# Optimization experiments

Measured on AMD Instinct MI355X. Metric: run time of the kernel, lower is better.

Reference implementation:

```python
import jax, jax.numpy as jnp
import numpy as np

N = 50000          # nodes
E = 800000         # edges per metapath
P = 4              # metapaths
IN = 256           # in_size
D = 32 * 8         # out_size * layer_num_heads = 256
SEM_H = 128        # SemanticAttention hidden


def setup_inputs() -> dict:
    key = jax.random.key(0)
    ks = jax.random.split(key, 8)
    h = jax.random.normal(ks[0], (N, IN), dtype=jnp.float32)
    src = jax.random.randint(ks[1], (P, E), 0, N, dtype=jnp.int32)
    dst = jax.random.randint(ks[2], (P, E), 0, N, dtype=jnp.int32)
    # per-metapath GraphConv weights (Glorot-ish scale)
    W_gc = jax.random.normal(ks[3], (P, IN, D), dtype=jnp.float32) / np.sqrt(IN)
    b_gc = jnp.zeros((P, D), dtype=jnp.float32)
    # SemanticAttention: Linear(D, SEM_H) -> tanh -> Linear(SEM_H, 1, bias=False)
    W1 = jax.random.normal(ks[4], (D, SEM_H), dtype=jnp.float32) / np.sqrt(D)
    b1 = jnp.zeros((SEM_H,), dtype=jnp.float32)
    w2 = jax.random.normal(ks[5], (SEM_H,), dtype=jnp.float32) / np.sqrt(SEM_H)
    return {"h": h, "src": src, "dst": dst, "W_gc": W_gc, "b_gc": b_gc,
            "W1": W1, "b1": b1, "w2": w2}


def _graph_conv(h, src, dst, W, b):
    # DGL GraphConv with norm='both': D_dst^{-1/2} A D_src^{-1/2} (h W) + b
    ones = jnp.ones((src.shape[0],), dtype=h.dtype)
    deg_out = jnp.clip(jax.ops.segment_sum(ones, src, num_segments=N), 1.0)
    deg_in = jnp.clip(jax.ops.segment_sum(ones, dst, num_segments=N), 1.0)
    x = (h @ W) * jax.lax.rsqrt(deg_out)[:, None]          # [N, D]
    agg = jax.ops.segment_sum(x[src], dst, num_segments=N)  # gather-scatter [N, D]
    return agg * jax.lax.rsqrt(deg_in)[:, None] + b


def reference(h, src, dst, W_gc, b_gc, W1, b1, w2):
    # per-metapath GraphConv (fixed small loop over P metapaths)
    zs = [_graph_conv(h, src[p], dst[p], W_gc[p], b_gc[p]) for p in range(P)]
    z = jnp.stack(zs, axis=1)                               # [N, P, D]
    # SemanticAttention: project -> mean over nodes -> softmax over metapaths
    s = jnp.tanh(z @ W1 + b1) @ w2                          # [N, P]
    beta = jax.nn.softmax(s.mean(axis=0), axis=0)           # [P]
    return jnp.einsum('npd,p->nd', z, beta)                 # [N, D]
```

## Files before the change

kernel.cpp:

```cpp
#include <hip/hip_runtime.h>

#define NN 50000
#define NE 800000
#define NP 4
#define DIN 256
#define DD 256
#define NH 128
#define SA 40
#define NSEG 16
#define SEGE (NE / NSEG)
#define HCH 32768
#define NHC 2
#define SCH 8192
#define NSC 7
#define SPAD(k) ((k) + ((k) >> 5))

typedef __attribute__((ext_vector_type(8))) short bf16x8;
typedef __attribute__((ext_vector_type(4))) float f32x4;
typedef __attribute__((ext_vector_type(2))) float f32x2;

__device__ __forceinline__ unsigned short f2bf(float f) {
  unsigned u = __float_as_uint(f);
  u += 0x7fff + ((u >> 16) & 1);
  return (unsigned short)(u >> 16);
}
__device__ __forceinline__ float bfl(unsigned u) { return __uint_as_float(u << 16); }
__device__ __forceinline__ float bfh(unsigned u) { return __uint_as_float(u & 0xffff0000u); }


__global__ __launch_bounds__(256) void histX_kernel(const int* __restrict__ src,
                                                    const int* __restrict__ dst,
                                                    ushort* __restrict__ cntS,
                                                    ushort* __restrict__ cntD) {
  __shared__ int hs[HCH];
  int bx = blockIdx.x;
  int c = bx % NHC, s = bx / NHC;
  int p = blockIdx.y;
  const int* idx = blockIdx.z ? dst : src;
  ushort* cnt = blockIdx.z ? cntD : cntS;
  int base = c * HCH, nk = min(HCH, NN - base);
  for (int k = threadIdx.x; k < HCH; k += 256) hs[k] = 0;
  __syncthreads();
  const int4* a4 = (const int4*)(idx + (size_t)p * NE + (size_t)s * SEGE);
  for (int i = threadIdx.x; i < SEGE / 4; i += 256) {
    int4 v = a4[i];
    int k;
    k = v.x - base; if ((unsigned)k < (unsigned)nk) atomicAdd(&hs[k], 1);
    k = v.y - base; if ((unsigned)k < (unsigned)nk) atomicAdd(&hs[k], 1);
    k = v.z - base; if ((unsigned)k < (unsigned)nk) atomicAdd(&hs[k], 1);
    k = v.w - base; if ((unsigned)k < (unsigned)nk) atomicAdd(&hs[k], 1);
  }
  __syncthreads();
  ushort* out = cnt + (size_t)(p * NSEG + s) * NN + base;
  for (int k = threadIdx.x; k < nk; k += 256) out[k] = (ushort)hs[k];
}


__global__ __launch_bounds__(1024) void scanA_kernel(
    ushort* __restrict__ cntD, const ushort* __restrict__ cntS,
    float* __restrict__ rin, float* __restrict__ rout,
    int* __restrict__ row_ptr, int* __restrict__ chunkdeg) {
  int c = blockIdx.x, p = blockIdx.y;
  int base = c * SCH, nk = min(SCH, NN - base);
  __shared__ int sdeg[SCH + (SCH >> 5)];
  __shared__ int wtot[16], wexc[16];
  int t = threadIdx.x;
  for (int kk = t; kk < SCH; kk += 1024) {
    int run = 0;
    if (kk < nk) {
      size_t o = (size_t)(p * NSEG) * NN + base + kk;
      int vD[NSEG], vS[NSEG];
#pragma unroll
      for (int s = 0; s < NSEG; ++s) vD[s] = cntD[o + (size_t)s * NN];
#pragma unroll
      for (int s = 0; s < NSEG; ++s) vS[s] = cntS[o + (size_t)s * NN];
#pragma unroll
      for (int s = 0; s < NSEG; ++s) {
        cntD[o + (size_t)s * NN] = (ushort)run;
        run += vD[s];
      }
      int rs = 0;
#pragma unroll
      for (int s = 0; s < NSEG; ++s) rs += vS[s];
      rin[(size_t)p * NN + base + kk] = rsqrtf((float)max(run, 1));
      rout[(size_t)p * NN + base + kk] = rsqrtf((float)max(rs, 1));
    }
    sdeg[SPAD(kk)] = run;
  }
  __syncthreads();
  int loc[8];
  int ssum = 0;
#pragma unroll
  for (int j = 0; j < 8; ++j) { loc[j] = ssum; ssum += sdeg[SPAD(t * 8 + j)]; }
  int incl = ssum;
  int lane = t & 63, w = t >> 6;
#pragma unroll
  for (int o = 1; o < 64; o <<= 1) {
    int v = __shfl_up(incl, o);
    if (lane >= o) incl += v;
  }
  if (lane == 63) wtot[w] = incl;
  __syncthreads();
  if (t == 0) {
    int r = 0;
    for (int i = 0; i < 16; ++i) { wexc[i] = r; r += wtot[i]; }
  }
  __syncthreads();
  int tbase = wexc[w] + incl - ssum;
  int* rp = row_ptr + (size_t)p * (NN + 1) + base;
#pragma unroll
  for (int j = 0; j < 8; ++j) {
    int k = t * 8 + j;
    if (k < nk) rp[k] = tbase + loc[j];
  }
  if (t == 1023) chunkdeg[p * NSC + c] = tbase + ssum;
}


__global__ __launch_bounds__(1024) void rpfin_kernel(int* __restrict__ row_ptr,
                                                     const int* __restrict__ chunkdeg) {
  int k = blockIdx.x * 1024 + threadIdx.x, p = blockIdx.y;
  if (k < NN) {
    int c = k >> 13;
    int cb = 0;
    for (int i = 0; i < c; ++i) cb += chunkdeg[p * NSC + i];
    row_ptr[(size_t)p * (NN + 1) + k] += cb;
  }
  if (k == 0) row_ptr[(size_t)p * (NN + 1) + NN] = NE;
}


__global__ __launch_bounds__(256) void scatter_kernel(
    const int* __restrict__ src, const int* __restrict__ dst,
    const ushort* __restrict__ cntD, const int* __restrict__ row_ptr, int* __restrict__ col) {
  __shared__ int cur[HCH];
  int bx = blockIdx.x;
  int c = bx % NHC, s = bx / NHC;
  int p = blockIdx.y;
  int base = c * HCH, nk = min(HCH, NN - base);
  for (int k = threadIdx.x; k < nk; k += 256)
    cur[k] = row_ptr[(size_t)p * (NN + 1) + base + k] +
             cntD[(size_t)(p * NSEG + s) * NN + base + k];
  __syncthreads();
  const int4* d4 = (const int4*)(dst + (size_t)p * NE + (size_t)s * SEGE);
  const int4* s4 = (const int4*)(src + (size_t)p * NE + (size_t)s * SEGE);
  int* colp = col + (size_t)p * NE;
  for (int i = threadIdx.x; i < SEGE / 4; i += 256) {
    int4 dv = d4[i];
    int4 sv = s4[i];
    int k;
    k = dv.x - base; if ((unsigned)k < (unsigned)nk) colp[atomicAdd(&cur[k], 1)] = sv.x;
    k = dv.y - base; if ((unsigned)k < (unsigned)nk) colp[atomicAdd(&cur[k], 1)] = sv.y;
    k = dv.z - base; if ((unsigned)k < (unsigned)nk) colp[atomicAdd(&cur[k], 1)] = sv.z;
    k = dv.w - base; if ((unsigned)k < (unsigned)nk) colp[atomicAdd(&cur[k], 1)] = sv.w;
  }
}


__global__ void cvt_h_kernel(const float4* __restrict__ h4, ushort4* __restrict__ h2) {
  int i = blockIdx.x * blockDim.x + threadIdx.x;
  if (i >= NN * DIN / 4) return;
  float4 v = h4[i];
  ushort4 o;
  o.x = f2bf(v.x); o.y = f2bf(v.y); o.z = f2bf(v.z); o.w = f2bf(v.w);
  h2[i] = o;
}


__global__ __launch_bounds__(256) void agg_kernel(
    const ushort* __restrict__ h2, const int* __restrict__ col,
    const int* __restrict__ row_ptr, const float* __restrict__ rout,
    const float* __restrict__ rin, ushort* __restrict__ g, int pbase) {
  __shared__ int2 sW[4][64];
  int p = pbase + blockIdx.y;
  int v = blockIdx.x * 4 + (threadIdx.x >> 6);
  int lane = threadIdx.x & 63;
  int wv = threadIdx.x >> 6;
  const int* colp = col + (size_t)p * NE;
  const float* rop = rout + (size_t)p * NN;
  int beg = row_ptr[p * (NN + 1) + v], end = row_ptr[p * (NN + 1) + v + 1];
  const char* hb = (const char*)h2 + (size_t)lane * 8;
  f32x2 accA0 = {0.f, 0.f}, accA1 = {0.f, 0.f};
  f32x2 accB0 = {0.f, 0.f}, accB1 = {0.f, 0.f};
  for (int j0 = beg; j0 < end; j0 += 64) {
    int nw = end - j0;
    if (nw > 64) nw = 64;
    int cv = 0;
    float rv = 0.f;
    if (lane < nw) { cv = colp[j0 + lane]; rv = rop[cv]; }
    sW[wv][lane] = make_int2(cv, __float_as_int(rv));
    int nwb = (nw + 7) & ~7;
    for (int t = 0; t < nwb; t += 8) {
      int2 w[8];
#pragma unroll
      for (int q = 0; q < 8; ++q) w[q] = sW[wv][t + q];
      uint2 u[8];
#pragma unroll
      for (int q = 0; q < 8; ++q)
        u[q] = *(const uint2*)(hb + ((size_t)(unsigned)w[q].x << 9));
#pragma unroll
      for (int q = 0; q < 8; ++q) {
        float r = __int_as_float(w[q].y);
        f32x2 rr = {r, r};
        if (q & 1) {
          asm("v_pk_fma_f32 %0, %1, %2, %0" : "+v"(accB0) : "v"(rr), "v"((f32x2){bfl(u[q].x), bfh(u[q].x)}));
          asm("v_pk_fma_f32 %0, %1, %2, %0" : "+v"(accB1) : "v"(rr), "v"((f32x2){bfl(u[q].y), bfh(u[q].y)}));
        } else {
          asm("v_pk_fma_f32 %0, %1, %2, %0" : "+v"(accA0) : "v"(rr), "v"((f32x2){bfl(u[q].x), bfh(u[q].x)}));
          asm("v_pk_fma_f32 %0, %1, %2, %0" : "+v"(accA1) : "v"(rr), "v"((f32x2){bfl(u[q].y), bfh(u[q].y)}));
        }
      }
    }
  }
  float ri = rin[(size_t)p * NN + v];
  f32x2 s0 = accA0 + accB0;
  f32x2 s1 = accA1 + accB1;
  ushort4 o;
  o.x = f2bf(s0.x * ri); o.y = f2bf(s0.y * ri);
  o.z = f2bf(s1.x * ri); o.w = f2bf(s1.y * ri);
  ((ushort4*)(g + ((size_t)p * NN + v) * DIN))[lane] = o;
}


__global__ void wmulcvec_kernel(const float* __restrict__ Wgc, const float* __restrict__ bgc,
                                const float* __restrict__ W1, const float* __restrict__ b1,
                                ushort* __restrict__ Mt, float* __restrict__ cvec) {
  int p = blockIdx.y, k = blockIdx.x, j = threadIdx.x;
  if (k < DIN) {
    const float* wrow = Wgc + ((size_t)p * DIN + k) * DD;
    float s = 0.f;
    for (int d = 0; d < DD; ++d) s = fmaf(wrow[d], W1[(size_t)d * NH + j], s);
    Mt[((size_t)p * NH + j) * DIN + k] = f2bf(s);
  } else {
    const float* b = bgc + (size_t)p * DD;
    float s = b1[j];
    for (int d = 0; d < DD; ++d) s = fmaf(b[d], W1[(size_t)d * NH + j], s);
    cvec[p * NH + j] = s;
  }
}


__global__ __launch_bounds__(256) void gemm_sem(
    const ushort* __restrict__ g, const ushort* __restrict__ Mt,
    const float* __restrict__ cvec, const float* __restrict__ w2,
    float* __restrict__ ssum) {
  __shared__ ushort As[128 * SA];
  __shared__ ushort Bs[128 * SA];
  __shared__ float wsumf[4];
  const int tid = threadIdx.x;
  const int p = blockIdx.y;
  const int row0 = blockIdx.x * 128;
  const int wave = tid >> 6, lane = tid & 63;
  const int wr = wave >> 1, wc = wave & 1;
  const int q = tid >> 2, sseg = tid & 3;
  const int srow = ((q & 31) << 1) | (q >> 5);
  const int fr = lane & 15, fk = (lane >> 4) * 8;
  const ushort* Ag = g + (size_t)p * NN * DIN;
  const ushort* Bg = Mt + (size_t)p * NH * DIN;
  int ar0 = row0 + srow; if (ar0 >= NN) ar0 = NN - 1;
  int ar1 = row0 + srow + 64; if (ar1 >= NN) ar1 = NN - 1;
  f32x4 acc[4][4] = {};
  for (int k2 = 0; k2 < DIN; k2 += 32) {
    uint4 av0 = *(const uint4*)(Ag + (size_t)ar0 * DIN + k2 + sseg * 8);
    uint4 av1 = *(const uint4*)(Ag + (size_t)ar1 * DIN + k2 + sseg * 8);
    uint4 bv0 = *(const uint4*)(Bg + (size_t)srow * DIN + k2 + sseg * 8);
    uint4 bv1 = *(const uint4*)(Bg + (size_t)(srow + 64) * DIN + k2 + sseg * 8);
    __syncthreads();
    *(uint4*)&As[srow * SA + sseg * 8] = av0;
    *(uint4*)&As[(srow + 64) * SA + sseg * 8] = av1;
    *(uint4*)&Bs[srow * SA + sseg * 8] = bv0;
    *(uint4*)&Bs[(srow + 64) * SA + sseg * 8] = bv1;
    __syncthreads();
    bf16x8 af[4], bfv[4];
#pragma unroll
    for (int t = 0; t < 4; ++t) {
      af[t] = *(const bf16x8*)&As[(wr * 64 + t * 16 + fr) * SA + fk];
      bfv[t] = *(const bf16x8*)&Bs[(wc * 64 + t * 16 + fr) * SA + fk];
    }
#pragma unroll
    for (int mt = 0; mt < 4; ++mt)
#pragma unroll
      for (int nt = 0; nt < 4; ++nt)
        acc[mt][nt] = __builtin_amdgcn_mfma_f32_16x16x32_bf16(af[mt], bfv[nt], acc[mt][nt], 0, 0, 0);
  }
  float s = 0.f;
#pragma unroll
  for (int nt = 0; nt < 4; ++nt) {
    int c = wc * 64 + nt * 16 + fr;
    float cc = cvec[p * NH + c];
    float ww = w2[c];
#pragma unroll
    for (int mt = 0; mt < 4; ++mt)
#pragma unroll
      for (int i = 0; i < 4; ++i) {
        int r = row0 + wr * 64 + mt * 16 + (lane >> 4) * 4 + i;
        if (r < NN) {
          float x = acc[mt][nt][i] + cc;
          x = fminf(fmaxf(x, -15.f), 15.f);
          float e = __expf(2.f * x);
          s = fmaf((e - 1.f) / (e + 1.f), ww, s);
        }
      }
  }
#pragma unroll
  for (int o = 32; o > 0; o >>= 1) s += __shfl_down(s, o);
  if (lane == 0) wsumf[wave] = s;
  __syncthreads();
  if (tid == 0) atomicAdd(&ssum[p], wsumf[0] + wsumf[1] + wsumf[2] + wsumf[3]);
}


__global__ __launch_bounds__(256) void scaleWtB_kernel(const float* __restrict__ Wgc,
                                                       const float* __restrict__ ssum,
                                                       const float* __restrict__ bgc,
                                                       ushort* __restrict__ Wt,
                                                       float* __restrict__ bout) {
  float m[NP];
  float mx = -1e30f;
#pragma unroll
  for (int p = 0; p < NP; ++p) {
    m[p] = ssum[p] * (1.f / (float)NN);
    mx = fmaxf(mx, m[p]);
  }
  float tot = 0.f;
#pragma unroll
  for (int p = 0; p < NP; ++p) { m[p] = __expf(m[p] - mx); tot += m[p]; }
  float inv = 1.f / tot;
  if (blockIdx.x == 0) {
    int d = threadIdx.x;
    float s = 0.f;
#pragma unroll
    for (int p = 0; p < NP; ++p) s = fmaf(m[p] * inv, bgc[p * DD + d], s);
    bout[d] = s;
  }
  int i = blockIdx.x * 256 + threadIdx.x;
  if (i < DD * NP * DIN) {
    int n = i >> 10;
    int pk = i & 1023;
    int p = pk >> 8, k = pk & 255;
    Wt[i] = f2bf(m[p] * inv * Wgc[((size_t)p * DIN + k) * DD + n]);
  }
}


__global__ __launch_bounds__(256) void gemm_main(
    const ushort* __restrict__ g, const ushort* __restrict__ Wt,
    const float* __restrict__ bout, float* __restrict__ out) {
  __shared__ ushort As[128 * SA];
  __shared__ ushort Bs[128 * SA];
  const int tid = threadIdx.x;
  const int row0 = blockIdx.y * 128;
  const int col0 = blockIdx.x * 128;
  const int wave = tid >> 6, lane = tid & 63;
  const int wr = wave >> 1, wc = wave & 1;
  const int q = tid >> 2, sseg = tid & 3;
  const int srow = ((q & 31) << 1) | (q >> 5);
  const int fr = lane & 15, fk = (lane >> 4) * 8;
  int ar0 = row0 + srow; if (ar0 >= NN) ar0 = NN - 1;
  int ar1 = row0 + srow + 64; if (ar1 >= NN) ar1 = NN - 1;
  f32x4 acc[4][4] = {};
  for (int p = 0; p < NP; ++p) {
    const ushort* Ag = g + (size_t)p * NN * DIN;
    for (int k2 = 0; k2 < DIN; k2 += 32) {
      uint4 av0 = *(const uint4*)(Ag + (size_t)ar0 * DIN + k2 + sseg * 8);
      uint4 av1 = *(const uint4*)(Ag + (size_t)ar1 * DIN + k2 + sseg * 8);
      uint4 bv0 = *(const uint4*)(Wt + (size_t)(col0 + srow) * (NP * DIN) + p * DIN + k2 + sseg * 8);
      uint4 bv1 = *(const uint4*)(Wt + (size_t)(col0 + srow + 64) * (NP * DIN) + p * DIN + k2 + sseg * 8);
      __syncthreads();
      *(uint4*)&As[srow * SA + sseg * 8] = av0;
      *(uint4*)&As[(srow + 64) * SA + sseg * 8] = av1;
      *(uint4*)&Bs[srow * SA + sseg * 8] = bv0;
      *(uint4*)&Bs[(srow + 64) * SA + sseg * 8] = bv1;
      __syncthreads();
      bf16x8 af[4], bfv[4];
#pragma unroll
      for (int t = 0; t < 4; ++t) {
        af[t] = *(const bf16x8*)&As[(wr * 64 + t * 16 + fr) * SA + fk];
        bfv[t] = *(const bf16x8*)&Bs[(wc * 64 + t * 16 + fr) * SA + fk];
      }
#pragma unroll
      for (int mt = 0; mt < 4; ++mt)
#pragma unroll
        for (int nt = 0; nt < 4; ++nt)
          acc[mt][nt] = __builtin_amdgcn_mfma_f32_16x16x32_bf16(af[mt], bfv[nt], acc[mt][nt], 0, 0, 0);
    }
  }
#pragma unroll
  for (int nt = 0; nt < 4; ++nt) {
    int c = col0 + wc * 64 + nt * 16 + fr;
    float bb = bout[c];
#pragma unroll
    for (int mt = 0; mt < 4; ++mt)
#pragma unroll
      for (int i = 0; i < 4; ++i) {
        int r = row0 + wr * 64 + mt * 16 + (lane >> 4) * 4 + i;
        if (r < NN) out[(size_t)r * DD + c] = acc[mt][nt][i] + bb;
      }
  }
}


extern "C" void kernel_launch(void* const* d_in, const int* in_sizes, int n_in,
                              void* d_out, int out_size, void* d_ws, size_t ws_size,
                              hipStream_t stream) {
  const float* h = (const float*)d_in[0];
  const int* src = (const int*)d_in[1];
  const int* dst = (const int*)d_in[2];
  const float* Wgc = (const float*)d_in[3];
  const float* bgc = (const float*)d_in[4];
  const float* W1 = (const float*)d_in[5];
  const float* b1 = (const float*)d_in[6];
  const float* w2 = (const float*)d_in[7];
  float* out = (float*)d_out;

  char* base = (char*)d_ws;
  size_t off = 0;
  auto alloc = [&](size_t bytes) -> char* {
    char* ptr = base + off;
    off = (off + bytes + 255) & ~(size_t)255;
    return ptr;
  };
  ushort* cntD = (ushort*)alloc((size_t)NP * NSEG * NN * sizeof(ushort));
  ushort* cntS = (ushort*)alloc((size_t)NP * NSEG * NN * sizeof(ushort));
  float* rin = (float*)alloc((size_t)NP * NN * sizeof(float));
  float* rout = (float*)alloc((size_t)NP * NN * sizeof(float));
  int* row_ptr = (int*)alloc((size_t)NP * (NN + 1) * sizeof(int));
  int* chunkdeg = (int*)alloc((size_t)NP * NSC * sizeof(int));
  int* colbuf = (int*)alloc((size_t)NP * NE * sizeof(int));
  ushort* h2 = (ushort*)alloc((size_t)NN * DIN * sizeof(ushort));
  ushort* g = (ushort*)alloc((size_t)NP * NN * DIN * sizeof(ushort));
  ushort* Mt = (ushort*)alloc((size_t)NP * NH * DIN * sizeof(ushort));
  ushort* Wt = (ushort*)alloc((size_t)DD * NP * DIN * sizeof(ushort));
  float* cvec = (float*)alloc((size_t)NP * NH * sizeof(float));
  float* ssum = (float*)alloc(NP * sizeof(float));
  float* bout = (float*)alloc(DD * sizeof(float));
  if (off > ws_size) return;

  hipMemsetAsync(ssum, 0, NP * sizeof(float), stream);

  histX_kernel<<<dim3(NHC * NSEG, NP, 2), 256, 0, stream>>>(src, dst, cntS, cntD);
  scanA_kernel<<<dim3(NSC, NP), 1024, 0, stream>>>(cntD, cntS, rin, rout, row_ptr, chunkdeg);
  rpfin_kernel<<<dim3((NN + 1023) / 1024, NP), 1024, 0, stream>>>(row_ptr, chunkdeg);
  cvt_h_kernel<<<(NN * DIN / 4 + 255) / 256, 256, 0, stream>>>((const float4*)h, (ushort4*)h2);
  scatter_kernel<<<dim3(NHC * NSEG, NP), 256, 0, stream>>>(src, dst, cntD, row_ptr, colbuf);
  agg_kernel<<<dim3(NN / 4, NP), 256, 0, stream>>>(h2, colbuf, row_ptr, rout, rin, g, 0);
  wmulcvec_kernel<<<dim3(DIN + 1, NP), NH, 0, stream>>>(Wgc, bgc, W1, b1, Mt, cvec);
  gemm_sem<<<dim3((NN + 127) / 128, NP), 256, 0, stream>>>(g, Mt, cvec, w2, ssum);
  scaleWtB_kernel<<<(DD * NP * DIN + 255) / 256, 256, 0, stream>>>(Wgc, ssum, bgc, Wt, bout);
  gemm_main<<<dim3(2, (NN + 127) / 128), 256, 0, stream>>>(g, Wt, bout, out);
}
```

Measured before the change: 575.0 us.

## Keep semantic-projection weights in registers and split aggregation launches per metapath

gemm_sem now drops shared-memory tiling. Each wave loads its 32-column slice of Mt into registers once, and a persistent grid of 512 blocks per metapath strides over 16-row groups, loading A fragments straight from global memory. This removes LDS staging and barriers and cuts repeated B loads, but it leaves less row reuse per A load. The agg kernel is also launched four times, one metapath each (using the last argument, presumably a metapath offset), instead of once with a y-grid of four. The likely aim is cache locality per metapath, at the cost of extra launch overhead.

Result: slower. 615.9 us (+7.1%).

```diff
diff --git a/kernel.cpp b/kernel.cpp
--- a/kernel.cpp
+++ b/kernel.cpp
@@ -244,63 +244,50 @@
     const ushort* __restrict__ g, const ushort* __restrict__ Mt,
     const float* __restrict__ cvec, const float* __restrict__ w2,
     float* __restrict__ ssum) {
-  __shared__ ushort As[128 * SA];
-  __shared__ ushort Bs[128 * SA];
   __shared__ float wsumf[4];
   const int tid = threadIdx.x;
   const int p = blockIdx.y;
-  const int row0 = blockIdx.x * 128;
   const int wave = tid >> 6, lane = tid & 63;
-  const int wr = wave >> 1, wc = wave & 1;
-  const int q = tid >> 2, sseg = tid & 3;
-  const int srow = ((q & 31) << 1) | (q >> 5);
   const int fr = lane & 15, fk = (lane >> 4) * 8;
   const ushort* Ag = g + (size_t)p * NN * DIN;
   const ushort* Bg = Mt + (size_t)p * NH * DIN;
-  int ar0 = row0 + srow; if (ar0 >= NN) ar0 = NN - 1;
-  int ar1 = row0 + srow + 64; if (ar1 >= NN) ar1 = NN - 1;
-  f32x4 acc[4][4] = {};
-  for (int k2 = 0; k2 < DIN; k2 += 32) {
-    uint4 av0 = *(const uint4*)(Ag + (size_t)ar0 * DIN + k2 + sseg * 8);
-    uint4 av1 = *(const uint4*)(Ag + (size_t)ar1 * DIN + k2 + sseg * 8);
-    uint4 bv0 = *(const uint4*)(Bg + (size_t)srow * DIN + k2 + sseg * 8);
-    uint4 bv1 = *(const uint4*)(Bg + (size_t)(srow + 64) * DIN + k2 + sseg * 8);
-    __syncthreads();
-    *(uint4*)&As[srow * SA + sseg * 8] = av0;
-    *(uint4*)&As[(srow + 64) * SA + sseg * 8] = av1;
-    *(uint4*)&Bs[srow * SA + sseg * 8] = bv0;
-    *(uint4*)&Bs[(srow + 64) * SA + sseg * 8] = bv1;
-    __syncthreads();
-    bf16x8 af[4], bfv[4];
-#pragma unroll
-    for (int t = 0; t < 4; ++t) {
-      af[t] = *(const bf16x8*)&As[(wr * 64 + t * 16 + fr) * SA + fk];
-      bfv[t] = *(const bf16x8*)&Bs[(wc * 64 + t * 16 + fr) * SA + fk];
+  bf16x8 bfv[2][8];
+#pragma unroll
+  for (int t = 0; t < 2; ++t)
+#pragma unroll
+    for (int ks = 0; ks < 8; ++ks)
+      bfv[t][ks] = *(const bf16x8*)(Bg + (size_t)(wave * 32 + t * 16 + fr) * DIN + ks * 32 + fk);
+  float cc[2], ww[2];
+#pragma unroll
+  for (int t = 0; t < 2; ++t) {
+    int c = wave * 32 + t * 16 + fr;
+    cc[t] = cvec[p * NH + c];
+    ww[t] = w2[c];
+  }
+  float s = 0.f;
+  for (int grp = blockIdx.x; grp < NN / 16; grp += gridDim.x) {
+    int row0 = grp * 16;
+    bf16x8 af[8];
+#pragma unroll
+    for (int ks = 0; ks < 8; ++ks)
+      af[ks] = *(const bf16x8*)(Ag + (size_t)(row0 + fr) * DIN + ks * 32 + fk);
+    f32x4 acc0 = {}, acc1 = {};
+#pragma unroll
+    for (int ks = 0; ks < 8; ++ks) {
+      acc0 = __builtin_amdgcn_mfma_f32_16x16x32_bf16(af[ks], bfv[0][ks], acc0, 0, 0, 0);
+      acc1 = __builtin_amdgcn_mfma_f32_16x16x32_bf16(af[ks], bfv[1][ks], acc1, 0, 0, 0);
     }
 #pragma unroll
-    for (int mt = 0; mt < 4; ++mt)
-#pragma unroll
-      for (int nt = 0; nt < 4; ++nt)
-        acc[mt][nt] = __builtin_amdgcn_mfma_f32_16x16x32_bf16(af[mt], bfv[nt], acc[mt][nt], 0, 0, 0);
-  }
-  float s = 0.f;
-#pragma unroll
-  for (int nt = 0; nt < 4; ++nt) {
-    int c = wc * 64 + nt * 16 + fr;
-    float cc = cvec[p * NH + c];
-    float ww = w2[c];
-#pragma unroll
-    for (int mt = 0; mt < 4; ++mt)
-#pragma unroll
-      for (int i = 0; i < 4; ++i) {
-        int r = row0 + wr * 64 + mt * 16 + (lane >> 4) * 4 + i;
-        if (r < NN) {
-          float x = acc[mt][nt][i] + cc;
-          x = fminf(fmaxf(x, -15.f), 15.f);
-          float e = __expf(2.f * x);
-          s = fmaf((e - 1.f) / (e + 1.f), ww, s);
-        }
-      }
+    for (int i = 0; i < 4; ++i) {
+      float x = acc0[i] + cc[0];
+      x = fminf(fmaxf(x, -15.f), 15.f);
+      float e = __expf(2.f * x);
+      s = fmaf((e - 1.f) / (e + 1.f), ww[0], s);
+      float y = acc1[i] + cc[1];
+      y = fminf(fmaxf(y, -15.f), 15.f);
+      float f = __expf(2.f * y);
+      s = fmaf((f - 1.f) / (f + 1.f), ww[1], s);
+    }
   }
 #pragma unroll
   for (int o = 32; o > 0; o >>= 1) s += __shfl_down(s, o);
@@ -443,9 +430,12 @@
   rpfin_kernel<<<dim3((NN + 1023) / 1024, NP), 1024, 0, stream>>>(row_ptr, chunkdeg);
   cvt_h_kernel<<<(NN * DIN / 4 + 255) / 256, 256, 0, stream>>>((const float4*)h, (ushort4*)h2);
   scatter_kernel<<<dim3(NHC * NSEG, NP), 256, 0, stream>>>(src, dst, cntD, row_ptr, colbuf);
-  agg_kernel<<<dim3(NN / 4, NP), 256, 0, stream>>>(h2, colbuf, row_ptr, rout, rin, g, 0);
+  agg_kernel<<<dim3(NN / 4, 1), 256, 0, stream>>>(h2, colbuf, row_ptr, rout, rin, g, 0);
+  agg_kernel<<<dim3(NN / 4, 1), 256, 0, stream>>>(h2, colbuf, row_ptr, rout, rin, g, 1);
+  agg_kernel<<<dim3(NN / 4, 1), 256, 0, stream>>>(h2, colbuf, row_ptr, rout, rin, g, 2);
+  agg_kernel<<<dim3(NN / 4, 1), 256, 0, stream>>>(h2, colbuf, row_ptr, rout, rin, g, 3);
   wmulcvec_kernel<<<dim3(DIN + 1, NP), NH, 0, stream>>>(Wgc, bgc, W1, b1, Mt, cvec);
-  gemm_sem<<<dim3((NN + 127) / 128, NP), 256, 0, stream>>>(g, Mt, cvec, w2, ssum);
+  gemm_sem<<<dim3(512, NP), 256, 0, stream>>>(g, Mt, cvec, w2, ssum);
   scaleWtB_kernel<<<(DD * NP * DIN + 255) / 256, 256, 0, stream>>>(Wgc, ssum, bgc, Wt, bout);
   gemm_main<<<dim3(2, (NN + 127) / 128), 256, 0, stream>>>(g, Wt, bout, out);
 }
```
